# Optimization experiments

Hardware: AMD Instinct MI355X
Metric: run time of the kernel (lower is better)

## Reference

```python
import jax, jax.numpy as jnp
import numpy as np

B, N, S = 8, 8192, 2048
IN, SKIP, OUT, EXP = 256, 128, 256, 4
GROUPS = 8


def conv1d(x, w, b):
    # 1x1 conv: x [B,C,N], w [O,C], b [O]
    return jnp.einsum('bcn,oc->bon', x, w) + b[None, :, None]


def group_norm(x, w, b, groups=GROUPS, eps=1e-5):
    Bb, C, Nn = x.shape
    xg = x.reshape(Bb, groups, C // groups, Nn)
    m = xg.mean(axis=(2, 3), keepdims=True)
    v = xg.var(axis=(2, 3), keepdims=True)
    xn = ((xg - m) * jax.lax.rsqrt(v + eps)).reshape(Bb, C, Nn)
    return xn * w[None, :, None] + b[None, :, None]


def _forward(xyz1, points1, xyz2, points2, t_emb, c_emb,
             mlp_w, mlp_b, mlp_gw, mlp_gb,
             c1w, c1b, g1w, g1b, c2w, c2b, g2w, g2b,
             tw, tb, cw, cb):
    # pairwise squared distances [B,N,S]
    dists = (-2.0 * jnp.einsum('bcn,bcm->bnm', xyz1, xyz2)
             + jnp.sum(xyz1 ** 2, axis=1)[:, :, None]
             + jnp.sum(xyz2 ** 2, axis=1)[:, None, :])
    neg_d3, idx = jax.lax.top_k(-dists, 3)          # 3 smallest distances
    d3 = -neg_d3                                     # [B,N,3]
    recip = 1.0 / (d3 + 1e-8)
    weight = recip / jnp.sum(recip, axis=2, keepdims=True)
    # gather neighbor features: points2 [B,C,S], idx [B,N,3] -> [B,C,N,3]
    gathered = jax.vmap(lambda p, i: p[:, i])(points2, idx)
    interp = jnp.sum(gathered * weight[:, None, :, :], axis=3)  # [B,IN,N]

    new_points = jnp.concatenate([points1, interp], axis=1)     # [B,IN+SKIP,N]
    x = jax.nn.silu(group_norm(conv1d(new_points, mlp_w, mlp_b), mlp_gw, mlp_gb))

    identity = x
    h = jax.nn.silu(group_norm(conv1d(x, c1w, c1b), g1w, g1b))
    h = group_norm(conv1d(h, c2w, c2b), g2w, g2b)
    st = t_emb @ tw.T + tb
    sc = c_emb @ cw.T + cb
    scale_t, shift_t = jnp.split(st, 2, axis=1)
    scale_c, shift_c = jnp.split(sc, 2, axis=1)
    scale = (scale_t + scale_c)[:, :, None]
    shift = (shift_t + shift_c)[:, :, None]
    h = h * (1.0 + scale) + shift
    return h + identity


def setup_inputs() -> dict:
    key = jax.random.key(0)
    ks = jax.random.split(key, 12)
    def rn(k, shape, s=1.0):
        return jax.random.normal(k, shape, dtype=jnp.float32) * s
    E = OUT * EXP
    return dict(
        xyz1=rn(ks[0], (B, 3, N)),
        points1=rn(ks[1], (B, SKIP, N)),
        xyz2=rn(ks[2], (B, 3, S)),
        points2=rn(ks[3], (B, IN, S)),
        t_emb=rn(ks[4], (B, OUT)),
        c_emb=rn(ks[5], (B, OUT)),
        mlp_w=rn(ks[6], (OUT, IN + SKIP), 0.02), mlp_b=jnp.zeros((OUT,), jnp.float32),
        mlp_gw=jnp.ones((OUT,), jnp.float32), mlp_gb=jnp.zeros((OUT,), jnp.float32),
        c1w=rn(ks[7], (E, OUT), 0.02), c1b=jnp.zeros((E,), jnp.float32),
        g1w=jnp.ones((E,), jnp.float32), g1b=jnp.zeros((E,), jnp.float32),
        c2w=rn(ks[8], (OUT, E), 0.02), c2b=jnp.zeros((OUT,), jnp.float32),
        g2w=jnp.ones((OUT,), jnp.float32), g2b=jnp.zeros((OUT,), jnp.float32),
        tw=rn(ks[9], (2 * OUT, OUT), 0.02), tb=jnp.zeros((2 * OUT,), jnp.float32),
        cw=rn(ks[10], (2 * OUT, OUT), 0.02), cb=jnp.zeros((2 * OUT,), jnp.float32),
    )


def reference(xyz1, points1, xyz2, points2, t_emb, c_emb,
              mlp_w, mlp_b, mlp_gw, mlp_gb,
              c1w, c1b, g1w, g1b, c2w, c2b, g2w, g2b,
              tw, tb, cw, cb):
    return _forward(xyz1, points1, xyz2, points2, t_emb, c_emb,
                    mlp_w, mlp_b, mlp_gw, mlp_gb,
                    c1w, c1b, g1w, g1b, c2w, c2b, g2w, g2b,
                    tw, tb, cw, cb)
```

## Files before the change

### kernel.cpp

```cpp
#include <hip/hip_runtime.h>
#include <hip/hip_bf16.h>

typedef unsigned short u16;
typedef __attribute__((ext_vector_type(4))) float f32x4;
typedef __attribute__((ext_vector_type(8))) short bf16x8;

typedef const __attribute__((address_space(1))) void GV;
typedef __attribute__((address_space(3))) void LV;
#define GLOAD16(g, l) __builtin_amdgcn_global_load_lds((GV*)(g), (LV*)(l), 16, 0, 0)

__device__ __forceinline__ float b2f(u16 u) {
    union { float f; unsigned int i; } v; v.i = ((unsigned int)u) << 16; return v.f;
}
__device__ __forceinline__ u16 f2b(float f) {
    union { float f; unsigned int i; } v; v.f = f;
    unsigned int x = v.i;
    return (u16)((x + 0x7fffu + ((x >> 16) & 1u)) >> 16);
}
__device__ __forceinline__ unsigned int cvt_pk_bf16(float lo, float hi) {
    unsigned int d;
    asm("v_cvt_pk_bf16_f32 %0, %1, %2" : "=v"(d) : "v"(lo), "v"(hi));
    return d;
}

__global__ void knn_part_kernel(const float* __restrict__ xyz1, const float* __restrict__ xyz2,
                                float2* __restrict__ cand) {
    __shared__ float4 spt[256];
    int b = blockIdx.z, ck = blockIdx.y, tid = threadIdx.x;
    const float* p2 = xyz2 + (size_t)b * 3 * 2048;
    int s0 = ck << 8;
    {
        int s = s0 + tid;
        float x = p2[s], y = p2[2048 + s], z = p2[4096 + s];
        spt[tid] = make_float4(x, y, z, (x * x + y * y) + z * z);
    }
    __syncthreads();
    int n = blockIdx.x * 256 + tid;
    const float* p1 = xyz1 + (size_t)b * 3 * 8192;
    float qx = p1[n], qy = p1[8192 + n], qz = p1[16384 + n];
    float qn = (qx * qx + qy * qy) + qz * qz;
    float d0 = 3.4e38f, d1 = 3.4e38f, d2 = 3.4e38f;
    int i0 = 0, i1 = 0, i2 = 0;
#pragma unroll 4
    for (int s = 0; s < 256; ++s) {
        float4 p = spt[s];
        float dot = (qx * p.x + qy * p.y) + qz * p.z;
        float d = (-2.f * dot + qn) + p.w;
        if (d < d2) {
            int gi = s0 + s;
            if (d < d1) {
                if (d < d0) { d2 = d1; i2 = i1; d1 = d0; i1 = i0; d0 = d; i0 = gi; }
                else        { d2 = d1; i2 = i1; d1 = d;  i1 = gi; }
            } else          { d2 = d;  i2 = gi; }
        }
    }
    float2* c = cand + (((size_t)b * 8192 + n) * 8 + ck) * 3;
    c[0] = make_float2(d0, __int_as_float(i0));
    c[1] = make_float2(d1, __int_as_float(i1));
    c[2] = make_float2(d2, __int_as_float(i2));
}

__global__ void knn_merge_kernel(const float2* __restrict__ cand,
                                 int* __restrict__ idx_out, float* __restrict__ w_out) {
    int t = blockIdx.x * 256 + threadIdx.x;
    const float2* c = cand + (size_t)t * 24;
    float d0 = 3.4e38f, d1 = 3.4e38f, d2 = 3.4e38f;
    int i0 = 0, i1 = 0, i2 = 0;
#pragma unroll
    for (int k = 0; k < 24; ++k) {
        float2 p = c[k];
        float d = p.x;
        if (d < d2) {
            int gi = __float_as_int(p.y);
            if (d < d1) {
                if (d < d0) { d2 = d1; i2 = i1; d1 = d0; i1 = i0; d0 = d; i0 = gi; }
                else        { d2 = d1; i2 = i1; d1 = d;  i1 = gi; }
            } else          { d2 = d;  i2 = gi; }
        }
    }
    float r0 = 1.f / (d0 + 1e-8f), r1 = 1.f / (d1 + 1e-8f), r2 = 1.f / (d2 + 1e-8f);
    float inv = 1.f / (r0 + r1 + r2);
    size_t base = (size_t)t * 3;
    idx_out[base] = i0; idx_out[base + 1] = i1; idx_out[base + 2] = i2;
    w_out[base] = r0 * inv; w_out[base + 1] = r1 * inv; w_out[base + 2] = r2 * inv;
}

__global__ void tr_kernel(const float* __restrict__ src, u16* __restrict__ dst, int C, int S) {
    __shared__ u16 tile[64][70];
    int b = blockIdx.z;
    int s0 = blockIdx.x * 64, c0 = blockIdx.y * 64;
    int tid = threadIdx.x, lane = tid & 63, wv = tid >> 6;
    const float* sp = src + ((size_t)b * C + c0) * S + s0;
    for (int c = wv; c < 64; c += 4)
        tile[lane][c] = f2b(sp[(size_t)c * S + lane]);
    __syncthreads();
    u16* dp = dst + ((size_t)b * S + s0) * C + c0;
    int s = tid >> 5, cp = tid & 31;
#pragma unroll
    for (int k = 0; k < 8; ++k) {
        int r = s + k * 8;
        unsigned int v = *(const unsigned int*)&tile[r][cp * 2];
        *(unsigned int*)&dp[(size_t)r * C + cp * 2] = v;
    }
}

__global__ void build_x0_kernel(const u16* __restrict__ p1t, const u16* __restrict__ p2t,
                                const int* __restrict__ idx, const float* __restrict__ wgt,
                                u16* __restrict__ x0t) {
    int b = blockIdx.y;
    int n = blockIdx.x * 64 + (threadIdx.x >> 2);
    int q = threadIdx.x & 3;
    size_t ib = ((size_t)b * 8192 + n) * 3;
    int j0 = idx[ib], j1 = idx[ib + 1], j2 = idx[ib + 2];
    float w0 = wgt[ib], w1 = wgt[ib + 1], w2 = wgt[ib + 2];
    const u16* pr = p1t + ((size_t)b * 8192 + n) * 128;
    const u16* r0 = p2t + ((size_t)b * 2048 + j0) * 256;
    const u16* r1 = p2t + ((size_t)b * 2048 + j1) * 256;
    const u16* r2 = p2t + ((size_t)b * 2048 + j2) * 256;
    u16* out = x0t + ((size_t)b * 8192 + n) * 384;
#pragma unroll
    for (int i = 0; i < 4; ++i) {
        int ch = (i * 4 + q) * 8;
        *(uint4*)&out[ch] = *(const uint4*)&pr[ch];
    }
#pragma unroll
    for (int i = 0; i < 8; ++i) {
        int c = (i * 4 + q) * 8;
        bf16x8 a0 = *(const bf16x8*)&r0[c];
        bf16x8 a1 = *(const bf16x8*)&r1[c];
        bf16x8 a2 = *(const bf16x8*)&r2[c];
        u16 ovu[8] __attribute__((aligned(16)));
#pragma unroll
        for (int j = 0; j < 8; ++j) {
            float v = w0 * b2f((u16)a0[j]) + w1 * b2f((u16)a1[j]) + w2 * b2f((u16)a2[j]);
            ovu[j] = f2b(v);
        }
        *(uint4*)&out[128 + c] = *(const uint4*)ovu;
    }
}

__global__ void cvt_kernel(const float* __restrict__ src, u16* __restrict__ dst, int n) {
    int i = blockIdx.x * 256 + threadIdx.x;
    if (i < n) dst[i] = f2b(src[i]);
}

__global__ void film_kernel(const float* __restrict__ t_emb, const float* __restrict__ c_emb,
                            const float* __restrict__ tw, const float* __restrict__ tb,
                            const float* __restrict__ cw, const float* __restrict__ cb,
                            float* __restrict__ film) {
    __shared__ float te[256], ce[256];
    int b = blockIdx.x, tid = threadIdx.x;
    te[tid] = t_emb[b * 256 + tid];
    ce[tid] = c_emb[b * 256 + tid];
    __syncthreads();
    int j = tid + blockIdx.y * 256;
    const float* twr = tw + (size_t)j * 256;
    const float* cwr = cw + (size_t)j * 256;
    float s = 0.f;
    for (int k = 0; k < 256; ++k) s += te[k] * twr[k] + ce[k] * cwr[k];
    s += tb[j] + cb[j];
    film[b * 512 + j] = s;
}

__global__ __launch_bounds__(512, 4) void gemm_kernel(
        const u16* __restrict__ At, const u16* __restrict__ W, const float* __restrict__ bias,
        u16* __restrict__ Out, float* __restrict__ part,
        int K, int M, int gshift) {
    __shared__ u16 lA[2][128 * 64];
    __shared__ u16 lB[2][128 * 64];
    __shared__ float bpart[4][2];
    int b = blockIdx.z;
    int n0 = blockIdx.x * 128, o0 = blockIdx.y * 128;
    int tid = threadIdx.x, lane = tid & 63, wv = tid >> 6;
    int wn = wv & 1;
    int wo = wv >> 1;
    if (tid < 8) ((float*)bpart)[tid] = 0.f;
    f32x4 acc[4][2];
#pragma unroll
    for (int i = 0; i < 4; i++)
#pragma unroll
        for (int j = 0; j < 2; j++) acc[i][j] = (f32x4){0.f, 0.f, 0.f, 0.f};

    int rl = lane >> 3;
    int csw = ((lane & 7) ^ rl) * 8;
    const u16* aP[2];
    const u16* bP[2];
#pragma unroll
    for (int p2 = 0; p2 < 2; p2++) {
        int p = wv * 2 + p2;
        aP[p2] = At + ((size_t)b * 8192 + n0 + p * 8 + rl) * K + csw;
        bP[p2] = W + ((size_t)(o0 + p * 8 + rl)) * K + csw;
    }
    int nK = K >> 6;
#pragma unroll
    for (int p2 = 0; p2 < 2; p2++) {
        int p = wv * 2 + p2;
        GLOAD16(aP[p2], &lA[0][p * 512]);
        GLOAD16(bP[p2], &lB[0][p * 512]);
        aP[p2] += 64; bP[p2] += 64;
    }
    asm volatile("s_waitcnt vmcnt(0) lgkmcnt(0)" ::: "memory");
    __builtin_amdgcn_s_barrier();
    int cur = 0;
    for (int kt = 0; kt < nK; ++kt) {
        if (kt + 1 < nK) {
#pragma unroll
            for (int p2 = 0; p2 < 2; p2++) {
                int p = wv * 2 + p2;
                GLOAD16(aP[p2], &lA[cur ^ 1][p * 512]);
                GLOAD16(bP[p2], &lB[cur ^ 1][p * 512]);
                aP[p2] += 64; bP[p2] += 64;
            }
        }
        const u16* la = lA[cur];
        const u16* lb = lB[cur];
#pragma unroll
        for (int kk = 0; kk < 2; kk++) {
            bf16x8 af[4], bfr[2];
#pragma unroll
            for (int mf = 0; mf < 4; mf++) {
                int R = wn * 64 + mf * 16 + (lane & 15);
                af[mf] = *(const bf16x8*)&la[R * 64 + ((kk * 4 + (lane >> 4)) ^ (R & 7)) * 8];
            }
#pragma unroll
            for (int nf = 0; nf < 2; nf++) {
                int R = wo * 32 + nf * 16 + (lane & 15);
                bfr[nf] = *(const bf16x8*)&lb[R * 64 + ((kk * 4 + (lane >> 4)) ^ (R & 7)) * 8];
            }
#pragma unroll
            for (int mf = 0; mf < 4; mf++)
#pragma unroll
                for (int nf = 0; nf < 2; nf++)
                    acc[mf][nf] = __builtin_amdgcn_mfma_f32_16x16x32_bf16(bfr[nf], af[mf], acc[mf][nf], 0, 0, 0);
        }
        if (kt + 1 < nK)
            asm volatile("s_waitcnt vmcnt(0)" ::: "memory");
        __builtin_amdgcn_s_barrier();
        cur ^= 1;
    }
    int oq = (lane >> 4) * 4;
    float4 bs[2];
    float s1[2] = {0.f, 0.f}, s2[2] = {0.f, 0.f};
#pragma unroll
    for (int nf = 0; nf < 2; nf++) bs[nf] = *(const float4*)&bias[o0 + wo * 32 + nf * 16 + oq];
#pragma unroll
    for (int mf = 0; mf < 4; mf++) {
        int n = n0 + wn * 64 + mf * 16 + (lane & 15);
        u16* rowp = Out + ((size_t)b * 8192 + n) * M + o0 + wo * 32 + oq;
#pragma unroll
        for (int nf = 0; nf < 2; nf++) {
            float v0 = acc[mf][nf][0] + bs[nf].x;
            float v1 = acc[mf][nf][1] + bs[nf].y;
            float v2 = acc[mf][nf][2] + bs[nf].z;
            float v3 = acc[mf][nf][3] + bs[nf].w;
            s1[nf] += (v0 + v1) + (v2 + v3);
            s2[nf] += (v0 * v0 + v1 * v1) + (v2 * v2 + v3 * v3);
            uint2 pk;
            pk.x = cvt_pk_bf16(v0, v1);
            pk.y = cvt_pk_bf16(v2, v3);
            *(uint2*)&rowp[nf * 16] = pk;
        }
    }
#pragma unroll
    for (int nf = 0; nf < 2; nf++) {
        float a = s1[nf], c = s2[nf];
#pragma unroll
        for (int off = 32; off > 0; off >>= 1) {
            a += __shfl_xor(a, off, 64);
            c += __shfl_xor(c, off, 64);
        }
        if (lane == 0) {
            int gl = (wo * 32 + nf * 16) >> gshift;
            atomicAdd(&bpart[gl][0], a);
            atomicAdd(&bpart[gl][1], c);
        }
    }
    __syncthreads();
    int nlg = 128 >> gshift;
    if (tid < 2 * nlg) {
        int gl = tid >> 1, s = tid & 1;
        int g = (o0 >> gshift) + gl;
        part[(((size_t)b * 8 + g) * 2 + s) * 64 + blockIdx.x] = bpart[gl][s];
    }
}

__global__ void gn_reduce_kernel(const float* __restrict__ part, float* __restrict__ stats) {
    int t = threadIdx.x;
    const float4* p = (const float4*)(part + (size_t)t * 64);
    float s = 0.f;
#pragma unroll
    for (int i = 0; i < 16; i++) { float4 v = p[i]; s += (v.x + v.y) + (v.z + v.w); }
    stats[t] = s;
}

__global__ void gn_act2_kernel(u16* __restrict__ Y, const float* __restrict__ gw,
                               const float* __restrict__ gb, const float* __restrict__ stats,
                               int c8bits, int gshift, float invCnt) {
    int t = blockIdx.x * 256 + threadIdx.x;
    int C8m = (1 << c8bits) - 1;
    int c8 = t & C8m;
    int c0 = c8 << 3;
    int g = c0 >> gshift;
    int row0 = t >> c8bits;
    int rowstep = (gridDim.x * 256) >> c8bits;
    float4 w0 = *(const float4*)(gw + c0), w1 = *(const float4*)(gw + c0 + 4);
    float4 b0 = *(const float4*)(gb + c0), b1 = *(const float4*)(gb + c0 + 4);
    float wv[8] = {w0.x, w0.y, w0.z, w0.w, w1.x, w1.y, w1.z, w1.w};
    float bv[8] = {b0.x, b0.y, b0.z, b0.w, b1.x, b1.y, b1.z, b1.w};
    float A[8], Bc[8];
    int bprev = -1;
    for (int row = row0; row < 65536; row += rowstep) {
        int b = row >> 13;
        if (b != bprev) {
            bprev = b;
            float sum = stats[(b * 8 + g) * 2], ssq = stats[(b * 8 + g) * 2 + 1];
            float m = sum * invCnt;
            float rstd = rsqrtf(fmaxf(ssq * invCnt - m * m, 0.f) + 1e-5f);
#pragma unroll
            for (int j = 0; j < 8; j++) { A[j] = rstd * wv[j]; Bc[j] = bv[j] - m * rstd * wv[j]; }
        }
        u16* p = Y + (((size_t)row << c8bits) << 3) + c0;
        uint4 v4 = *(const uint4*)p;
        u16* vu = (u16*)&v4;
#pragma unroll
        for (int j = 0; j < 8; j++) {
            float v = b2f(vu[j]) * A[j] + Bc[j];
            v = v * __builtin_amdgcn_rcpf(1.f + __expf(-v));
            vu[j] = f2b(v);
        }
        *(uint4*)p = v4;
    }
}

__global__ void final_kernel(const u16* __restrict__ Y2, const u16* __restrict__ X,
                             const float* __restrict__ g2w, const float* __restrict__ g2b,
                             const float* __restrict__ stats, const float* __restrict__ film,
                             float* __restrict__ out) {
    __shared__ float tile[64][257];
    int b = blockIdx.y, n0 = blockIdx.x * 64, tid = threadIdx.x;
    const float invCnt = 1.f / (32.f * 8192.f);
    int c8 = tid & 31, c0 = c8 << 3, g = c8 >> 2;
    float sum = stats[(b * 8 + g) * 2], ssq = stats[(b * 8 + g) * 2 + 1];
    float m = sum * invCnt, rstd = rsqrtf(fmaxf(ssq * invCnt - m * m, 0.f) + 1e-5f);
    float4 w0 = *(const float4*)(g2w + c0), w1 = *(const float4*)(g2w + c0 + 4);
    float4 q0 = *(const float4*)(g2b + c0), q1 = *(const float4*)(g2b + c0 + 4);
    float4 f0 = *(const float4*)(film + b * 512 + c0), f1 = *(const float4*)(film + b * 512 + c0 + 4);
    float4 h0 = *(const float4*)(film + b * 512 + 256 + c0), h1 = *(const float4*)(film + b * 512 + 256 + c0 + 4);
    float wv[8] = {w0.x, w0.y, w0.z, w0.w, w1.x, w1.y, w1.z, w1.w};
    float qv[8] = {q0.x, q0.y, q0.z, q0.w, q1.x, q1.y, q1.z, q1.w};
    float fs[8] = {f0.x, f0.y, f0.z, f0.w, f1.x, f1.y, f1.z, f1.w};
    float fh[8] = {h0.x, h0.y, h0.z, h0.w, h1.x, h1.y, h1.z, h1.w};
    float A[8], Bc[8];
#pragma unroll
    for (int j = 0; j < 8; j++) {
        float sc = 1.f + fs[j];
        A[j] = rstd * wv[j] * sc;
        Bc[j] = (qv[j] - m * rstd * wv[j]) * sc + fh[j];
    }
    int nrb = tid >> 5;
#pragma unroll
    for (int k = 0; k < 8; k++) {
        int nr = nrb + k * 8;
        size_t base = ((size_t)b * 8192 + n0 + nr) * 256 + c0;
        uint4 yv = *(const uint4*)(Y2 + base);
        uint4 xv = *(const uint4*)(X + base);
        const u16* yy = (const u16*)&yv;
        const u16* xx = (const u16*)&xv;
#pragma unroll
        for (int j = 0; j < 8; j++)
            tile[nr][c0 + j] = b2f(yy[j]) * A[j] + Bc[j] + b2f(xx[j]);
    }
    __syncthreads();
    for (int q = tid; q < 256 * 16; q += 256) {
        int c = q >> 4, n4 = q & 15;
        float4 o;
        o.x = tile[n4 * 4 + 0][c];
        o.y = tile[n4 * 4 + 1][c];
        o.z = tile[n4 * 4 + 2][c];
        o.w = tile[n4 * 4 + 3][c];
        *(float4*)&out[((size_t)b * 256 + c) * 8192 + n0 + n4 * 4] = o;
    }
}

extern "C" void kernel_launch(void* const* d_in, const int* in_sizes, int n_in,
                              void* d_out, int out_size, void* d_ws, size_t ws_size,
                              hipStream_t stream) {
    const float* xyz1    = (const float*)d_in[0];
    const float* points1 = (const float*)d_in[1];
    const float* xyz2    = (const float*)d_in[2];
    const float* points2 = (const float*)d_in[3];
    const float* t_emb   = (const float*)d_in[4];
    const float* c_emb   = (const float*)d_in[5];
    const float* mlp_w   = (const float*)d_in[6];
    const float* mlp_b   = (const float*)d_in[7];
    const float* mlp_gw  = (const float*)d_in[8];
    const float* mlp_gb  = (const float*)d_in[9];
    const float* c1w     = (const float*)d_in[10];
    const float* c1b     = (const float*)d_in[11];
    const float* g1w     = (const float*)d_in[12];
    const float* g1b     = (const float*)d_in[13];
    const float* c2w     = (const float*)d_in[14];
    const float* c2b     = (const float*)d_in[15];
    const float* g2w     = (const float*)d_in[16];
    const float* g2b     = (const float*)d_in[17];
    const float* tw      = (const float*)d_in[18];
    const float* tb      = (const float*)d_in[19];
    const float* cw      = (const float*)d_in[20];
    const float* cb      = (const float*)d_in[21];

    char* ws = (char*)d_ws;
    int*   idx    = (int*)ws;
    float* wgt    = (float*)(ws + 786432);
    float* stats0 = (float*)(ws + 1572864);
    float* stats1 = (float*)(ws + 1573376);
    float* stats2 = (float*)(ws + 1573888);
    float* film   = (float*)(ws + 1574400);
    float* part0  = (float*)(ws + 1590784);
    float* part1  = (float*)(ws + 1623552);
    float* part2  = (float*)(ws + 1656320);
    u16* wb_mlp   = (u16*)(ws + 1689088);
    u16* wb_c1    = (u16*)(ws + 1885696);
    u16* wb_c2    = (u16*)(ws + 2409984);
    u16* X0t = (u16*)(ws + 4194304);
    u16* Y1t = (u16*)(ws + 54525952);
    u16* H1t = (u16*)(ws + 88080384);
    u16* Y2t = X0t;
    float2* cand = (float2*)X0t;
    u16* p1t = H1t;
    u16* p2t = H1t + 8388608ull;
    float* out = (float*)d_out;

    cvt_kernel<<<384, 256, 0, stream>>>(mlp_w, wb_mlp, 98304);
    cvt_kernel<<<1024, 256, 0, stream>>>(c1w, wb_c1, 262144);
    cvt_kernel<<<1024, 256, 0, stream>>>(c2w, wb_c2, 262144);
    knn_part_kernel<<<dim3(32, 8, 8), 256, 0, stream>>>(xyz1, xyz2, cand);
    knn_merge_kernel<<<256, 256, 0, stream>>>(cand, idx, wgt);
    tr_kernel<<<dim3(128, 2, 8), 256, 0, stream>>>(points1, p1t, 128, 8192);
    tr_kernel<<<dim3(32, 4, 8), 256, 0, stream>>>(points2, p2t, 256, 2048);
    build_x0_kernel<<<dim3(128, 8), 256, 0, stream>>>(p1t, p2t, idx, wgt, X0t);
    film_kernel<<<dim3(8, 2), 256, 0, stream>>>(t_emb, c_emb, tw, tb, cw, cb, film);
    gemm_kernel<<<dim3(64, 2, 8), 512, 0, stream>>>(X0t, wb_mlp, mlp_b, Y1t, part0, 384, 256, 5);
    gn_reduce_kernel<<<1, 128, 0, stream>>>(part0, stats0);
    gn_act2_kernel<<<512, 256, 0, stream>>>(Y1t, mlp_gw, mlp_gb, stats0, 5, 5, 1.f / (32.f * 8192.f));
    gemm_kernel<<<dim3(64, 8, 8), 512, 0, stream>>>(Y1t, wb_c1, c1b, H1t, part1, 256, 1024, 7);
    gn_reduce_kernel<<<1, 128, 0, stream>>>(part1, stats1);
    gn_act2_kernel<<<2048, 256, 0, stream>>>(H1t, g1w, g1b, stats1, 7, 7, 1.f / (128.f * 8192.f));
    gemm_kernel<<<dim3(64, 2, 8), 512, 0, stream>>>(H1t, wb_c2, c2b, Y2t, part2, 1024, 256, 5);
    gn_reduce_kernel<<<1, 128, 0, stream>>>(part2, stats2);
    final_kernel<<<dim3(128, 8), 256, 0, stream>>>(Y2t, Y1t, g2w, g2b, stats2, film, out);
}
```

Baseline: 379.8 us.

## Fuse GroupNorm+SiLU into next GEMM's A-operand load, drop in-place activation passes

Removes the two standalone gn_act2 passes that read and rewrote the bf16 activations in place. Per-batch, per-channel scale/shift tables are now computed by a tiny gn_coef kernel. A new gemm_gn_kernel applies normalize+SiLU to A tiles in registers before staging them into LDS, and the final kernel recomputes the first GroupNorm+SiLU on the residual path. This saves two full read/write passes over large intermediates (Y1 and H1, the latter 1024 channels wide). In exchange the A path moves from async global-to-LDS loads to register loads plus ALU work inside the GEMM loop, and SiLU is recomputed for each output tile block (8 times for the c1 GEMM).

Result: no change. 374.2 us (-1.5%).

```diff
diff --git a/kernel.cpp b/kernel.cpp
--- a/kernel.cpp
+++ b/kernel.cpp
@@ -21,6 +21,9 @@
     unsigned int d;
     asm("v_cvt_pk_bf16_f32 %0, %1, %2" : "=v"(d) : "v"(lo), "v"(hi));
     return d;
+}
+__device__ __forceinline__ float silu(float t) {
+    return t * __builtin_amdgcn_rcpf(1.f + __expf(-t));
 }
 
 __global__ void knn_part_kernel(const float* __restrict__ xyz1, const float* __restrict__ xyz2,
@@ -172,8 +175,7 @@
     int b = blockIdx.z;
     int n0 = blockIdx.x * 128, o0 = blockIdx.y * 128;
     int tid = threadIdx.x, lane = tid & 63, wv = tid >> 6;
-    int wn = wv & 1;
-    int wo = wv >> 1;
+    int wn = wv & 1, wo = wv >> 1;
     if (tid < 8) ((float*)bpart)[tid] = 0.f;
     f32x4 acc[4][2];
 #pragma unroll
@@ -284,6 +286,174 @@
     }
 }
 
+__global__ __launch_bounds__(512, 4) void gemm_gn_kernel(
+        const u16* __restrict__ At, const u16* __restrict__ W, const float* __restrict__ bias,
+        const float* __restrict__ tab,
+        u16* __restrict__ Out, float* __restrict__ part,
+        int K, int M, int gshift) {
+    __shared__ u16 lA[2][128 * 64];
+    __shared__ u16 lB[2][128 * 64];
+    __shared__ float cA[1024], cB[1024];
+    __shared__ float bpart[4][2];
+    int b = blockIdx.z;
+    int n0 = blockIdx.x * 128, o0 = blockIdx.y * 128;
+    int tid = threadIdx.x, lane = tid & 63, wv = tid >> 6;
+    int wn = wv & 1, wo = wv >> 1;
+    if (tid < 8) ((float*)bpart)[tid] = 0.f;
+    f32x4 acc[4][2];
+#pragma unroll
+    for (int i = 0; i < 4; i++)
+#pragma unroll
+        for (int j = 0; j < 2; j++) acc[i][j] = (f32x4){0.f, 0.f, 0.f, 0.f};
+
+    int rl = lane >> 3;
+    int csw = ((lane & 7) ^ rl) * 8;
+    const u16* aP[2];
+    const u16* bP[2];
+#pragma unroll
+    for (int p2 = 0; p2 < 2; p2++) {
+        int p = wv * 2 + p2;
+        aP[p2] = At + ((size_t)b * 8192 + n0 + p * 8 + rl) * K + csw;
+        bP[p2] = W + ((size_t)(o0 + p * 8 + rl)) * K + csw;
+    }
+    int nK = K >> 6;
+    uint4 areg[2];
+#pragma unroll
+    for (int p2 = 0; p2 < 2; p2++) { areg[p2] = *(const uint4*)aP[p2]; aP[p2] += 64; }
+#pragma unroll
+    for (int p2 = 0; p2 < 2; p2++) {
+        int p = wv * 2 + p2;
+        GLOAD16(bP[p2], &lB[0][p * 512]);
+        bP[p2] += 64;
+    }
+    {
+        const float* tA = tab + (size_t)b * K;
+        const float* tB = tab + (size_t)(8 + b) * K;
+        for (int i = tid; i < K; i += 512) { cA[i] = tA[i]; cB[i] = tB[i]; }
+    }
+    __syncthreads();
+#pragma unroll
+    for (int p2 = 0; p2 < 2; p2++) {
+        int p = wv * 2 + p2;
+        int c = csw;
+        const u16* rr = (const u16*)&areg[p2];
+        float4 a0 = *(const float4*)&cA[c], a1 = *(const float4*)&cA[c + 4];
+        float4 b0 = *(const float4*)&cB[c], b1 = *(const float4*)&cB[c + 4];
+        float va[8] = {a0.x, a0.y, a0.z, a0.w, a1.x, a1.y, a1.z, a1.w};
+        float vb[8] = {b0.x, b0.y, b0.z, b0.w, b1.x, b1.y, b1.z, b1.w};
+        float v[8];
+#pragma unroll
+        for (int j = 0; j < 8; ++j) v[j] = silu(b2f(rr[j]) * va[j] + vb[j]);
+        uint4 o;
+        o.x = cvt_pk_bf16(v[0], v[1]); o.y = cvt_pk_bf16(v[2], v[3]);
+        o.z = cvt_pk_bf16(v[4], v[5]); o.w = cvt_pk_bf16(v[6], v[7]);
+        *(uint4*)&lA[0][p * 512 + lane * 8] = o;
+    }
+    asm volatile("s_waitcnt vmcnt(0) lgkmcnt(0)" ::: "memory");
+    __builtin_amdgcn_s_barrier();
+    int cur = 0;
+    for (int kt = 0; kt < nK; ++kt) {
+        if (kt + 1 < nK) {
+#pragma unroll
+            for (int p2 = 0; p2 < 2; p2++) { areg[p2] = *(const uint4*)aP[p2]; aP[p2] += 64; }
+#pragma unroll
+            for (int p2 = 0; p2 < 2; p2++) {
+                int p = wv * 2 + p2;
+                GLOAD16(bP[p2], &lB[cur ^ 1][p * 512]);
+                bP[p2] += 64;
+            }
+        }
+        const u16* la = lA[cur];
+        const u16* lb = lB[cur];
+#pragma unroll
+        for (int kk = 0; kk < 2; kk++) {
+            bf16x8 af[4], bfr[2];
+#pragma unroll
+            for (int mf = 0; mf < 4; mf++) {
+                int R = wn * 64 + mf * 16 + (lane & 15);
+                af[mf] = *(const bf16x8*)&la[R * 64 + ((kk * 4 + (lane >> 4)) ^ (R & 7)) * 8];
+            }
+#pragma unroll
+            for (int nf = 0; nf < 2; nf++) {
+                int R = wo * 32 + nf * 16 + (lane & 15);
+                bfr[nf] = *(const bf16x8*)&lb[R * 64 + ((kk * 4 + (lane >> 4)) ^ (R & 7)) * 8];
+            }
+#pragma unroll
+            for (int mf = 0; mf < 4; mf++)
+#pragma unroll
+                for (int nf = 0; nf < 2; nf++)
+                    acc[mf][nf] = __builtin_amdgcn_mfma_f32_16x16x32_bf16(bfr[nf], af[mf], acc[mf][nf], 0, 0, 0);
+        }
+        if (kt + 1 < nK) {
+            int c = (kt + 1) * 64 + csw;
+            float4 a0 = *(const float4*)&cA[c], a1 = *(const float4*)&cA[c + 4];
+            float4 b0 = *(const float4*)&cB[c], b1 = *(const float4*)&cB[c + 4];
+            float va[8] = {a0.x, a0.y, a0.z, a0.w, a1.x, a1.y, a1.z, a1.w};
+            float vb[8] = {b0.x, b0.y, b0.z, b0.w, b1.x, b1.y, b1.z, b1.w};
+#pragma unroll
+            for (int p2 = 0; p2 < 2; p2++) {
+                int p = wv * 2 + p2;
+                const u16* rr = (const u16*)&areg[p2];
+                float v[8];
+#pragma unroll
+                for (int j = 0; j < 8; ++j) v[j] = silu(b2f(rr[j]) * va[j] + vb[j]);
+                uint4 o;
+                o.x = cvt_pk_bf16(v[0], v[1]); o.y = cvt_pk_bf16(v[2], v[3]);
+                o.z = cvt_pk_bf16(v[4], v[5]); o.w = cvt_pk_bf16(v[6], v[7]);
+                *(uint4*)&lA[cur ^ 1][p * 512 + lane * 8] = o;
+            }
+            asm volatile("s_waitcnt vmcnt(0)" ::: "memory");
+        }
+        asm volatile("s_waitcnt lgkmcnt(0)" ::: "memory");
+        __builtin_amdgcn_s_barrier();
+        cur ^= 1;
+    }
+    int oq = (lane >> 4) * 4;
+    float4 bs[2];
+    float s1[2] = {0.f, 0.f}, s2[2] = {0.f, 0.f};
+#pragma unroll
+    for (int nf = 0; nf < 2; nf++) bs[nf] = *(const float4*)&bias[o0 + wo * 32 + nf * 16 + oq];
+#pragma unroll
+    for (int mf = 0; mf < 4; mf++) {
+        int n = n0 + wn * 64 + mf * 16 + (lane & 15);
+        u16* rowp = Out + ((size_t)b * 8192 + n) * M + o0 + wo * 32 + oq;
+#pragma unroll
+        for (int nf = 0; nf < 2; nf++) {
+            float v0 = acc[mf][nf][0] + bs[nf].x;
+            float v1 = acc[mf][nf][1] + bs[nf].y;
+            float v2 = acc[mf][nf][2] + bs[nf].z;
+            float v3 = acc[mf][nf][3] + bs[nf].w;
+            s1[nf] += (v0 + v1) + (v2 + v3);
+            s2[nf] += (v0 * v0 + v1 * v1) + (v2 * v2 + v3 * v3);
+            uint2 pk;
+            pk.x = cvt_pk_bf16(v0, v1);
+            pk.y = cvt_pk_bf16(v2, v3);
+            *(uint2*)&rowp[nf * 16] = pk;
+        }
+    }
+#pragma unroll
+    for (int nf = 0; nf < 2; nf++) {
+        float a = s1[nf], c = s2[nf];
+#pragma unroll
+        for (int off = 32; off > 0; off >>= 1) {
+            a += __shfl_xor(a, off, 64);
+            c += __shfl_xor(c, off, 64);
+        }
+        if (lane == 0) {
+            int gl = (wo * 32 + nf * 16) >> gshift;
+            atomicAdd(&bpart[gl][0], a);
+            atomicAdd(&bpart[gl][1], c);
+        }
+    }
+    __syncthreads();
+    int nlg = 128 >> gshift;
+    if (tid < 2 * nlg) {
+        int gl = tid >> 1, s = tid & 1;
+        int g = (o0 >> gshift) + gl;
+        part[(((size_t)b * 8 + g) * 2 + s) * 64 + blockIdx.x] = bpart[gl][s];
+    }
+}
+
 __global__ void gn_reduce_kernel(const float* __restrict__ part, float* __restrict__ stats) {
     int t = threadIdx.x;
     const float4* p = (const float4*)(part + (size_t)t * 64);
@@ -293,69 +463,54 @@
     stats[t] = s;
 }
 
-__global__ void gn_act2_kernel(u16* __restrict__ Y, const float* __restrict__ gw,
-                               const float* __restrict__ gb, const float* __restrict__ stats,
-                               int c8bits, int gshift, float invCnt) {
-    int t = blockIdx.x * 256 + threadIdx.x;
-    int C8m = (1 << c8bits) - 1;
-    int c8 = t & C8m;
-    int c0 = c8 << 3;
-    int g = c0 >> gshift;
-    int row0 = t >> c8bits;
-    int rowstep = (gridDim.x * 256) >> c8bits;
-    float4 w0 = *(const float4*)(gw + c0), w1 = *(const float4*)(gw + c0 + 4);
-    float4 b0 = *(const float4*)(gb + c0), b1 = *(const float4*)(gb + c0 + 4);
-    float wv[8] = {w0.x, w0.y, w0.z, w0.w, w1.x, w1.y, w1.z, w1.w};
-    float bv[8] = {b0.x, b0.y, b0.z, b0.w, b1.x, b1.y, b1.z, b1.w};
-    float A[8], Bc[8];
-    int bprev = -1;
-    for (int row = row0; row < 65536; row += rowstep) {
-        int b = row >> 13;
-        if (b != bprev) {
-            bprev = b;
-            float sum = stats[(b * 8 + g) * 2], ssq = stats[(b * 8 + g) * 2 + 1];
-            float m = sum * invCnt;
-            float rstd = rsqrtf(fmaxf(ssq * invCnt - m * m, 0.f) + 1e-5f);
-#pragma unroll
-            for (int j = 0; j < 8; j++) { A[j] = rstd * wv[j]; Bc[j] = bv[j] - m * rstd * wv[j]; }
-        }
-        u16* p = Y + (((size_t)row << c8bits) << 3) + c0;
-        uint4 v4 = *(const uint4*)p;
-        u16* vu = (u16*)&v4;
-#pragma unroll
-        for (int j = 0; j < 8; j++) {
-            float v = b2f(vu[j]) * A[j] + Bc[j];
-            v = v * __builtin_amdgcn_rcpf(1.f + __expf(-v));
-            vu[j] = f2b(v);
-        }
-        *(uint4*)p = v4;
-    }
-}
-
-__global__ void final_kernel(const u16* __restrict__ Y2, const u16* __restrict__ X,
+__global__ void gn_coef_kernel(const float* __restrict__ stats, const float* __restrict__ gw,
+                               const float* __restrict__ gb, float* __restrict__ tab,
+                               int K, int gshift, float invCnt) {
+    int c = blockIdx.x * 256 + threadIdx.x;
+    int b = blockIdx.y;
+    int g = c >> gshift;
+    float sum = stats[(b * 8 + g) * 2], ssq = stats[(b * 8 + g) * 2 + 1];
+    float m = sum * invCnt;
+    float rstd = rsqrtf(fmaxf(ssq * invCnt - m * m, 0.f) + 1e-5f);
+    float A = rstd * gw[c];
+    tab[(size_t)b * K + c] = A;
+    tab[(size_t)(8 + b) * K + c] = gb[c] - m * A;
+}
+
+__global__ void final_kernel(const u16* __restrict__ Y2, const u16* __restrict__ Xraw,
+                             const float* __restrict__ g0w, const float* __restrict__ g0b,
+                             const float* __restrict__ stats0,
                              const float* __restrict__ g2w, const float* __restrict__ g2b,
-                             const float* __restrict__ stats, const float* __restrict__ film,
+                             const float* __restrict__ stats2, const float* __restrict__ film,
                              float* __restrict__ out) {
     __shared__ float tile[64][257];
     int b = blockIdx.y, n0 = blockIdx.x * 64, tid = threadIdx.x;
     const float invCnt = 1.f / (32.f * 8192.f);
     int c8 = tid & 31, c0 = c8 << 3, g = c8 >> 2;
-    float sum = stats[(b * 8 + g) * 2], ssq = stats[(b * 8 + g) * 2 + 1];
+    float sum = stats2[(b * 8 + g) * 2], ssq = stats2[(b * 8 + g) * 2 + 1];
     float m = sum * invCnt, rstd = rsqrtf(fmaxf(ssq * invCnt - m * m, 0.f) + 1e-5f);
+    float sum0 = stats0[(b * 8 + g) * 2], ssq0 = stats0[(b * 8 + g) * 2 + 1];
+    float m0 = sum0 * invCnt, rstd0 = rsqrtf(fmaxf(ssq0 * invCnt - m0 * m0, 0.f) + 1e-5f);
     float4 w0 = *(const float4*)(g2w + c0), w1 = *(const float4*)(g2w + c0 + 4);
     float4 q0 = *(const float4*)(g2b + c0), q1 = *(const float4*)(g2b + c0 + 4);
     float4 f0 = *(const float4*)(film + b * 512 + c0), f1 = *(const float4*)(film + b * 512 + c0 + 4);
     float4 h0 = *(const float4*)(film + b * 512 + 256 + c0), h1 = *(const float4*)(film + b * 512 + 256 + c0 + 4);
+    float4 u0 = *(const float4*)(g0w + c0), u1 = *(const float4*)(g0w + c0 + 4);
+    float4 e0 = *(const float4*)(g0b + c0), e1 = *(const float4*)(g0b + c0 + 4);
     float wv[8] = {w0.x, w0.y, w0.z, w0.w, w1.x, w1.y, w1.z, w1.w};
     float qv[8] = {q0.x, q0.y, q0.z, q0.w, q1.x, q1.y, q1.z, q1.w};
     float fs[8] = {f0.x, f0.y, f0.z, f0.w, f1.x, f1.y, f1.z, f1.w};
     float fh[8] = {h0.x, h0.y, h0.z, h0.w, h1.x, h1.y, h1.z, h1.w};
-    float A[8], Bc[8];
+    float uv[8] = {u0.x, u0.y, u0.z, u0.w, u1.x, u1.y, u1.z, u1.w};
+    float ev[8] = {e0.x, e0.y, e0.z, e0.w, e1.x, e1.y, e1.z, e1.w};
+    float A[8], Bc[8], A0[8], B0[8];
 #pragma unroll
     for (int j = 0; j < 8; j++) {
         float sc = 1.f + fs[j];
         A[j] = rstd * wv[j] * sc;
         Bc[j] = (qv[j] - m * rstd * wv[j]) * sc + fh[j];
+        A0[j] = rstd0 * uv[j];
+        B0[j] = ev[j] - m0 * A0[j];
     }
     int nrb = tid >> 5;
 #pragma unroll
@@ -363,12 +518,14 @@
         int nr = nrb + k * 8;
         size_t base = ((size_t)b * 8192 + n0 + nr) * 256 + c0;
         uint4 yv = *(const uint4*)(Y2 + base);
-        uint4 xv = *(const uint4*)(X + base);
+        uint4 xv = *(const uint4*)(Xraw + base);
         const u16* yy = (const u16*)&yv;
         const u16* xx = (const u16*)&xv;
 #pragma unroll
-        for (int j = 0; j < 8; j++)
-            tile[nr][c0 + j] = b2f(yy[j]) * A[j] + Bc[j] + b2f(xx[j]);
+        for (int j = 0; j < 8; j++) {
+            float x = silu(b2f(xx[j]) * A0[j] + B0[j]);
+            tile[nr][c0 + j] = b2f(yy[j]) * A[j] + Bc[j] + x;
+        }
     }
     __syncthreads();
     for (int q = tid; q < 256 * 16; q += 256) {
@@ -421,6 +578,8 @@
     u16* wb_mlp   = (u16*)(ws + 1689088);
     u16* wb_c1    = (u16*)(ws + 1885696);
     u16* wb_c2    = (u16*)(ws + 2409984);
+    float* tab0   = (float*)(ws + 2934272);
+    float* tab1   = (float*)(ws + 2950656);
     u16* X0t = (u16*)(ws + 4194304);
     u16* Y1t = (u16*)(ws + 54525952);
     u16* H1t = (u16*)(ws + 88080384);
@@ -441,11 +600,12 @@
     film_kernel<<<dim3(8, 2), 256, 0, stream>>>(t_emb, c_emb, tw, tb, cw, cb, film);
     gemm_kernel<<<dim3(64, 2, 8), 512, 0, stream>>>(X0t, wb_mlp, mlp_b, Y1t, part0, 384, 256, 5);
     gn_reduce_kernel<<<1, 128, 0, stream>>>(part0, stats0);
-    gn_act2_kernel<<<512, 256, 0, stream>>>(Y1t, mlp_gw, mlp_gb, stats0, 5, 5, 1.f / (32.f * 8192.f));
-    gemm_kernel<<<dim3(64, 8, 8), 512, 0, stream>>>(Y1t, wb_c1, c1b, H1t, part1, 256, 1024, 7);
+    gn_coef_kernel<<<dim3(1, 8), 256, 0, stream>>>(stats0, mlp_gw, mlp_gb, tab0, 256, 5, 1.f / (32.f * 8192.f));
+    gemm_gn_kernel<<<dim3(64, 8, 8), 512, 0, stream>>>(Y1t, wb_c1, c1b, tab0, H1t, part1, 256, 1024, 7);
     gn_reduce_kernel<<<1, 128, 0, stream>>>(part1, stats1);
-    gn_act2_kernel<<<2048, 256, 0, stream>>>(H1t, g1w, g1b, stats1, 7, 7, 1.f / (128.f * 8192.f));
-    gemm_kernel<<<dim3(64, 2, 8), 512, 0, stream>>>(H1t, wb_c2, c2b, Y2t, part2, 1024, 256, 5);
+    gn_coef_kernel<<<dim3(4, 8), 256, 0, stream>>>(stats1, g1w, g1b, tab1, 1024, 7, 1.f / (128.f * 8192.f));
+    gemm_gn_kernel<<<dim3(64, 2, 8), 512, 0, stream>>>(H1t, wb_c2, c2b, tab1, Y2t, part2, 1024, 256, 5);
     gn_reduce_kernel<<<1, 128, 0, stream>>>(part2, stats2);
-    final_kernel<<<dim3(128, 8), 256, 0, stream>>>(Y2t, Y1t, g2w, g2b, stats2, film, out);
-}
+    final_kernel<<<dim3(128, 8), 256, 0, stream>>>(Y2t, Y1t, mlp_gw, mlp_gb, stats0,
+                                                   g2w, g2b, stats2, film, out);
+}
```
